# Optimization experiments

Hardware: AMD Instinct MI355X
Metric: run time of the kernel (lower is better)

The kernel has to match this reference:

```python
import jax, jax.numpy as jnp
import numpy as np

EPS = 1e-5
DIL = 2
PAD = 2  # dilation * (kernel_size - 1) // 2


def _conv(x, w, dil, pad):
    return jax.lax.conv_general_dilated(
        x, w, window_strides=(1, 1), padding=[(pad, pad), (pad, pad)],
        rhs_dilation=(dil, dil), dimension_numbers=('NCHW', 'OIHW', 'NCHW'))


def _bn(x, g, b):
    # BatchNorm2d in training mode: per-channel batch stats over (N,H,W)
    m = x.mean(axis=(0, 2, 3), keepdims=True)
    v = x.var(axis=(0, 2, 3), keepdims=True)
    return (x - m) * jax.lax.rsqrt(v + EPS) * g[None, :, None, None] + b[None, :, None, None]


def _deform_conv(x, offset, w, dil=DIL, pad=PAD):
    # torchvision deform_conv2d v1 (no modulation): offset [B, 2*K, H, W] with
    # channel ordering (dy_0, dx_0, dy_1, dx_1, ...), kernel tap k = ky*3 + kx.
    B, C, H, W = x.shape
    Co = w.shape[0]
    K = 9
    off = offset.reshape(B, K, 2, H, W)
    dy, dx = off[:, :, 0], off[:, :, 1]              # [B,K,H,W]
    kr = jnp.arange(3)
    kyy = (jnp.repeat(kr, 3) * dil - pad).astype(x.dtype)   # [K]
    kxx = (jnp.tile(kr, 3) * dil - pad).astype(x.dtype)     # [K]
    hg = jnp.arange(H, dtype=x.dtype)
    wg = jnp.arange(W, dtype=x.dtype)
    py = hg[None, None, :, None] + kyy[None, :, None, None] + dy   # [B,K,H,W]
    px = wg[None, None, None, :] + kxx[None, :, None, None] + dx   # [B,K,H,W]
    y0 = jnp.floor(py)
    x0 = jnp.floor(px)
    wy = py - y0   # [B,K,H,W]
    wx = px - x0
    y0i = y0.astype(jnp.int32)
    x0i = x0.astype(jnp.int32)
    x_flat = x.reshape(B, C, H * W)

    def corner(yi, xi):
        valid = ((yi >= 0) & (yi < H) & (xi >= 0) & (xi < W)).astype(x.dtype)  # [B,K,H,W]
        idx = jnp.clip(yi, 0, H - 1) * W + jnp.clip(xi, 0, W - 1)
        v = jax.vmap(lambda xb, ib: xb[:, ib])(x_flat, idx.reshape(B, -1))    # [B,C,K*H*W]
        return v.reshape(B, C, K, H, W) * valid[:, None]

    v00 = corner(y0i, x0i)
    v01 = corner(y0i, x0i + 1)
    v10 = corner(y0i + 1, x0i)
    v11 = corner(y0i + 1, x0i + 1)
    wy_ = wy[:, None]   # [B,1,K,H,W]
    wx_ = wx[:, None]
    sampled = (v00 * (1 - wy_) * (1 - wx_) + v01 * (1 - wy_) * wx_
               + v10 * wy_ * (1 - wx_) + v11 * wy_ * wx_)          # [B,C,K,H,W]
    return jnp.einsum('bckhw,ock->bohw', sampled, w.reshape(Co, C, K))


def setup_inputs() -> dict:
    key = jax.random.key(0)
    ks = jax.random.split(key, 4)
    B, C, H, W = 4, 256, 56, 56
    x = jax.random.normal(ks[0], (B, C, H, W), dtype=jnp.float32)
    w_off = jax.random.normal(ks[1], (18, C, 3, 3), dtype=jnp.float32) * 0.01
    b_off = jnp.zeros((18,), dtype=jnp.float32)
    w1 = jax.random.normal(ks[2], (C, C, 3, 3), dtype=jnp.float32) * (1.0 / np.sqrt(9 * C))
    w2 = jax.random.normal(ks[3], (C, C, 3, 3), dtype=jnp.float32) * (1.0 / np.sqrt(9 * C))
    gamma1 = jnp.ones((C,), dtype=jnp.float32)
    beta1 = jnp.zeros((C,), dtype=jnp.float32)
    gamma2 = jnp.ones((C,), dtype=jnp.float32)
    beta2 = jnp.zeros((C,), dtype=jnp.float32)
    return {'x': x, 'w_off': w_off, 'b_off': b_off, 'w1': w1, 'gamma1': gamma1,
            'beta1': beta1, 'w2': w2, 'gamma2': gamma2, 'beta2': beta2}


def reference(x, w_off, b_off, w1, gamma1, beta1, w2, gamma2, beta2):
    offset = _conv(x, w_off, DIL, PAD) + b_off[None, :, None, None]   # [B,18,H,W]
    out = _deform_conv(x, offset, w1)
    out = jax.nn.relu(_bn(out, gamma1, beta1))
    out = _conv(out, w2, 1, 1)
    out = _bn(out, gamma2, beta2)
    return jax.nn.relu(out + x)
```

## Files before the change

### kernel.cpp

```cpp
#include <hip/hip_runtime.h>

typedef __bf16 bf16;
typedef bf16 bf16x4 __attribute__((ext_vector_type(4)));
typedef bf16 bf16x8 __attribute__((ext_vector_type(8)));
typedef float f32x4 __attribute__((ext_vector_type(4)));

#define CH 256
#define HH 56
#define WW 56
#define HW 3136
#define MM 12544
#define KT 2304

__device__ __forceinline__ void gll16(const bf16* g, bf16* l) {
  __builtin_amdgcn_global_load_lds(
      (const __attribute__((address_space(1))) void*)g,
      (__attribute__((address_space(3))) void*)l, 16, 0, 0);
}

template <int N>
__device__ __forceinline__ void waitvm() {
  if constexpr (N == 0) asm volatile("s_waitcnt vmcnt(0)" ::: "memory");
  else if constexpr (N == 3) asm volatile("s_waitcnt vmcnt(3)" ::: "memory");
  else if constexpr (N == 4) asm volatile("s_waitcnt vmcnt(4)" ::: "memory");
}

__global__ __launch_bounds__(256) void nchw2nhwc_k(const float* __restrict__ x,
                                                   bf16* __restrict__ o) {
  __shared__ float t[32][33];
  const int b = blockIdx.z, hw0 = blockIdx.x * 32, c0 = blockIdx.y * 32;
  const int tid = threadIdx.x;
  {
    const int cl = tid >> 3, hwl = (tid & 7) * 4;
    f32x4 v = *(const f32x4*)&x[(size_t)(b * CH + c0 + cl) * HW + hw0 + hwl];
#pragma unroll
    for (int i = 0; i < 4; ++i) t[cl][hwl + i] = v[i];
  }
  __syncthreads();
  const int hwl = tid >> 3, cl = (tid & 7) * 4;
  bf16x4 ov;
#pragma unroll
  for (int i = 0; i < 4; ++i) ov[i] = (bf16)t[cl + i][hwl];
  *(bf16x4*)&o[(size_t)(b * HW + hw0 + hwl) * CH + c0 + cl] = ov;
}

__global__ void reorder_all_k(const float* __restrict__ w1,
                              const float* __restrict__ w2,
                              const float* __restrict__ woff,
                              bf16* __restrict__ w1t, bf16* __restrict__ w2t,
                              bf16* __restrict__ wof) {
  const int gid = blockIdx.x;
  if (gid < 4608) {
    const int idx = gid * 256 + threadIdx.x;
    const float* in = (gid < 2304) ? w1 : w2;
    bf16* out = (gid < 2304) ? w1t : w2t;
    const int li = (gid < 2304) ? idx : idx - 2304 * 256;
    const int o = li / KT, r = li - o * KT;
    const int k = r >> 8, c = r & 255;
    out[li] = (bf16)in[(size_t)(o * CH + c) * 9 + k];
  } else {
    const int li = (gid - 4608) * 256 + threadIdx.x;
    const int o = li / KT, r = li - o * KT;
    const int k = r >> 8, c = r & 255;
    wof[li] = (bf16)((o < 18) ? woff[(size_t)(o * CH + c) * 9 + k] : 0.f);
  }
}

__global__ __launch_bounds__(256) void build_deform_k(
    const bf16* __restrict__ xn, const float* __restrict__ offb,
    const float* __restrict__ boff, bf16* __restrict__ A1) {
  const int tid = threadIdx.x;
  const int m = blockIdx.x * 16 + (tid >> 4);
  const int l15 = tid & 15;
  const int b = m / HW, hw = m - b * HW;
  const int h = hw / WW, w = hw - h * WW;
  const float* orow = offb + m * 18;
  const bf16* xb = xn + (size_t)b * HW * CH;
  bf16* dst = A1 + (size_t)m * KT;
  for (int tap = 0; tap < 9; ++tap) {
    const int ky = tap / 3, kx = tap - ky * 3;
    const float dy = orow[2 * tap] + boff[2 * tap];
    const float dx = orow[2 * tap + 1] + boff[2 * tap + 1];
    const float py = (float)(h + ky * 2 - 2) + dy;
    const float px = (float)(w + kx * 2 - 2) + dx;
    const float y0f = floorf(py), x0f = floorf(px);
    const int y0 = (int)y0f, x0 = (int)x0f;
    const float wy = py - y0f, wx = px - x0f;
    const float w00 = (1.f - wy) * (1.f - wx), w01 = (1.f - wy) * wx;
    const float w10 = wy * (1.f - wx), w11 = wy * wx;
    const bool vy0 = (unsigned)y0 < HH, vy1 = (unsigned)(y0 + 1) < HH;
    const bool vx0 = (unsigned)x0 < WW, vx1 = (unsigned)(x0 + 1) < WW;
    const bf16* p00 = xb + (long long)(y0 * WW + x0) * CH;
#pragma unroll
    for (int j = 0; j < 2; ++j) {
      const int cc = j * 128 + l15 * 8;
      bf16x8 v00 = {}, v01 = {}, v10 = {}, v11 = {};
      if (vy0 && vx0) v00 = *(const bf16x8*)(p00 + cc);
      if (vy0 && vx1) v01 = *(const bf16x8*)(p00 + CH + cc);
      if (vy1 && vx0) v10 = *(const bf16x8*)(p00 + WW * CH + cc);
      if (vy1 && vx1) v11 = *(const bf16x8*)(p00 + WW * CH + CH + cc);
      bf16x8 o;
#pragma unroll
      for (int i = 0; i < 8; ++i)
        o[i] = (bf16)(w00 * (float)v00[i] + w01 * (float)v01[i] +
                      w10 * (float)v10[i] + w11 * (float)v11[i]);
      *(bf16x8*)(dst + tap * 256 + cc) = o;
    }
  }
}

template <int MODE, int EPI, int SWZ, int TN, int KS>
__global__ __launch_bounds__(256, 3) void gemm_k(
    const bf16* __restrict__ Asrc, const bf16* __restrict__ Bt,
    const bf16* __restrict__ zp, bf16* __restrict__ outb,
    float* __restrict__ sS, float* __restrict__ sQ,
    float* __restrict__ offout, const int dil, const int pad) {
  constexpr int PB = TN / 32;
  constexpr int NF = TN / 32;
  constexpr int SL = 2 + PB;
  __shared__ __align__(16) bf16 Ab[2][4096];
  __shared__ __align__(16) bf16 Bb[2][TN * 64];
  const int tid = threadIdx.x;
  int n0, m0;
  if (SWZ) {
    const int gid = blockIdx.x;
    const int swz = (gid & 7) * 98 + (gid >> 3);
    n0 = (swz & 3) * 64;
    m0 = (swz >> 2) * 64;
  } else {
    n0 = blockIdx.x * TN;
    m0 = blockIdx.y * 64;
  }
  const int kbase = blockIdx.z * KS * 64;
  const int lane = tid & 63, wv = tid >> 6;
  const int wrM = wv >> 1, wcN = wv & 1;
  const int fr = lane & 15, kg = lane >> 4;
  const int srow = tid >> 3, cpos = tid & 7;
  const int sxor = (cpos ^ (srow & 7)) * 8;

  int bb[2], hh[2], wwv[2];
  const bf16* aptr[2];
  if (MODE == 1) {
#pragma unroll
    for (int pa = 0; pa < 2; ++pa) {
      const int m = m0 + pa * 32 + srow;
      bb[pa] = m / HW;
      const int hw = m - bb[pa] * HW;
      hh[pa] = hw / WW;
      wwv[pa] = hw - hh[pa] * WW;
    }
  } else {
#pragma unroll
    for (int pa = 0; pa < 2; ++pa)
      aptr[pa] = Asrc + (size_t)(m0 + pa * 32 + srow) * KT + kbase + sxor;
  }
  const bf16* bptr[PB];
#pragma unroll
  for (int pb = 0; pb < PB; ++pb)
    bptr[pb] = Bt + (size_t)(n0 + pb * 32 + srow) * KT + kbase + sxor;

  f32x4 acc[2][NF] = {};

  auto STAGE = [&](int kt, int buf) {
    const int kk = kbase + kt * 64;
#pragma unroll
    for (int pa = 0; pa < 2; ++pa) {
      const bf16* as;
      if (MODE == 0) {
        as = aptr[pa] + kt * 64;
      } else {
        const int tap = kk >> 8, coff = kk & 255;
        const int ky = tap / 3, kx = tap - ky * 3;
        const int y = hh[pa] + ky * dil - pad, xx = wwv[pa] + kx * dil - pad;
        const bool ok = ((unsigned)y < HH) && ((unsigned)xx < WW);
        as = ok ? Asrc + ((size_t)(bb[pa] * HW + y * WW + xx) * CH + coff + sxor)
                : zp + sxor;
      }
      gll16(as, &Ab[buf][(pa * 32 + srow) * 64 + cpos * 8]);
    }
#pragma unroll
    for (int pb = 0; pb < PB; ++pb)
      gll16(bptr[pb] + kt * 64, &Bb[buf][(pb * 32 + srow) * 64 + cpos * 8]);
  };

  auto COMPUTE = [&](int buf) {
#pragma unroll
    for (int kh = 0; kh < 2; ++kh) {
      bf16x8 af[2], bv[NF];
#pragma unroll
      for (int mf = 0; mf < 2; ++mf) {
        const int row = wrM * 32 + mf * 16 + fr;
        const int g = (kh * 4 + kg) ^ (row & 7);
        af[mf] = *(const bf16x8*)&Ab[buf][row * 64 + g * 8];
      }
#pragma unroll
      for (int nf = 0; nf < NF; ++nf) {
        const int row = wcN * (NF * 16) + nf * 16 + fr;
        const int g = (kh * 4 + kg) ^ (row & 7);
        bv[nf] = *(const bf16x8*)&Bb[buf][row * 64 + g * 8];
      }
#pragma unroll
      for (int mf = 0; mf < 2; ++mf)
#pragma unroll
        for (int nf = 0; nf < NF; ++nf)
          acc[mf][nf] = __builtin_amdgcn_mfma_f32_16x16x32_bf16(af[mf], bv[nf],
                                                                acc[mf][nf], 0, 0, 0);
    }
  };

  STAGE(0, 0);
  STAGE(1, 1);
  int buf = 0;
  for (int kt = 0; kt < KS; ++kt) {
    if (kt + 1 < KS) waitvm<SL>();
    else waitvm<0>();
    __builtin_amdgcn_s_barrier();
    __builtin_amdgcn_sched_barrier(0);
    COMPUTE(buf);
    __builtin_amdgcn_sched_barrier(0);
    __builtin_amdgcn_s_barrier();
    if (kt + 2 < KS) STAGE(kt + 2, buf);
    buf ^= 1;
  }

  if constexpr (EPI == 1) {
#pragma unroll
    for (int mf = 0; mf < 2; ++mf) {
      const int rr = m0 + wrM * 32 + mf * 16 + kg * 4;
#pragma unroll
      for (int nf = 0; nf < NF; ++nf) {
        const int col = n0 + wcN * (NF * 16) + nf * 16 + fr;
#pragma unroll
        for (int r = 0; r < 4; ++r)
          outb[(size_t)(rr + r) * CH + col] = (bf16)acc[mf][nf][r];
      }
    }
    float ps[NF], pq[NF];
#pragma unroll
    for (int nf = 0; nf < NF; ++nf) {
      float s = 0.f, q = 0.f;
#pragma unroll
      for (int mf = 0; mf < 2; ++mf)
#pragma unroll
        for (int r = 0; r < 4; ++r) {
          const float v = acc[mf][nf][r];
          s += v;
          q += v * v;
        }
      s += __shfl_xor(s, 16);
      s += __shfl_xor(s, 32);
      q += __shfl_xor(q, 16);
      q += __shfl_xor(q, 32);
      ps[nf] = s;
      pq[nf] = q;
    }
    float* red = (float*)&Ab[0][0];
    if (tid < 128) red[tid] = 0.f;
    __syncthreads();
    if (kg == 0) {
#pragma unroll
      for (int nf = 0; nf < NF; ++nf) {
        const int cb = wcN * (NF * 16) + nf * 16 + fr;
        atomicAdd(&red[cb], ps[nf]);
        atomicAdd(&red[64 + cb], pq[nf]);
      }
    }
    __syncthreads();
    if (tid < 64) {
      atomicAdd(&sS[n0 + tid], red[tid]);
      atomicAdd(&sQ[n0 + tid], red[64 + tid]);
    }
  } else {
#pragma unroll
    for (int mf = 0; mf < 2; ++mf) {
      const int rr = m0 + wrM * 32 + mf * 16 + kg * 4;
#pragma unroll
      for (int nf = 0; nf < NF; ++nf) {
        const int col = n0 + wcN * (NF * 16) + nf * 16 + fr;
        if (col < 18) {
#pragma unroll
          for (int r = 0; r < 4; ++r)
            atomicAdd(&offout[(size_t)(rr + r) * 18 + col], acc[mf][nf][r]);
        }
      }
    }
  }
}

__global__ __launch_bounds__(256) void a1_kb(const bf16* __restrict__ in,
                                             const float* __restrict__ s,
                                             const float* __restrict__ sq,
                                             const float* __restrict__ g,
                                             const float* __restrict__ be,
                                             bf16* __restrict__ out) {
  const size_t idx = (size_t)(blockIdx.x * 256 + threadIdx.x) * 8;
  const int c0 = (int)(idx & 255);
  const float inv = 1.f / (float)MM;
  bf16x8 v = *(const bf16x8*)&in[idx];
  bf16x8 o;
#pragma unroll
  for (int i = 0; i < 8; ++i) {
    const int c = c0 + i;
    const float mean = s[c] * inv;
    const float var = sq[c] * inv - mean * mean;
    const float sc = g[c] * rsqrtf(var + 1e-5f);
    const float bi = be[c] - mean * sc;
    float r = (float)v[i] * sc + bi;
    o[i] = (bf16)(r > 0.f ? r : 0.f);
  }
  *(bf16x8*)&out[idx] = o;
}

__global__ __launch_bounds__(256) void final_kb(const bf16* __restrict__ o2,
                                                const float* __restrict__ x,
                                                const float* __restrict__ s,
                                                const float* __restrict__ sq,
                                                const float* __restrict__ g,
                                                const float* __restrict__ be,
                                                float* __restrict__ out) {
  __shared__ float t[32][33];
  const int b = blockIdx.z, hw0 = blockIdx.x * 32, o0 = blockIdx.y * 32;
  const int tid = threadIdx.x;
  {
    const int hwl = tid >> 3, ol = (tid & 7) * 4;
    bf16x4 v = *(const bf16x4*)&o2[(size_t)(b * HW + hw0 + hwl) * CH + o0 + ol];
#pragma unroll
    for (int i = 0; i < 4; ++i) t[ol + i][hwl] = (float)v[i];
  }
  __syncthreads();
  const int ol = tid >> 3, hwl = (tid & 7) * 4;
  const int ch = o0 + ol;
  const float inv = 1.f / (float)MM;
  const float mean = s[ch] * inv;
  const float var = sq[ch] * inv - mean * mean;
  const float sc = g[ch] * rsqrtf(var + 1e-5f);
  const float bb = be[ch] - mean * sc;
  const size_t xi = (size_t)(b * CH + ch) * HW + hw0 + hwl;
  f32x4 xv = *(const f32x4*)&x[xi];
  f32x4 r;
#pragma unroll
  for (int i = 0; i < 4; ++i) {
    float v = t[ol][hwl + i] * sc + bb + xv[i];
    r[i] = v > 0.f ? v : 0.f;
  }
  *(f32x4*)&out[xi] = r;
}

#define WS_XN 0ULL
#define WS_W1T 6422528ULL
#define WS_W2T 7602176ULL
#define WS_WOF 8781824ULL
#define WS_OFFB 9076736ULL
#define WS_A1 9979904ULL
#define WS_O1 67782656ULL
#define WS_ACT 74205184ULL
#define WS_O2 80627712ULL
#define WS_ZP 87050240ULL
#define WS_STAT 87054336ULL

extern "C" void kernel_launch(void* const* d_in, const int* in_sizes, int n_in,
                              void* d_out, int out_size, void* d_ws, size_t ws_size,
                              hipStream_t stream) {
  const float* x = (const float*)d_in[0];
  const float* w_off = (const float*)d_in[1];
  const float* b_off = (const float*)d_in[2];
  const float* w1 = (const float*)d_in[3];
  const float* g1 = (const float*)d_in[4];
  const float* be1 = (const float*)d_in[5];
  const float* w2 = (const float*)d_in[6];
  const float* g2 = (const float*)d_in[7];
  const float* be2 = (const float*)d_in[8];
  float* out = (float*)d_out;
  char* ws = (char*)d_ws;

  bf16* xn = (bf16*)(ws + WS_XN);
  bf16* w1t = (bf16*)(ws + WS_W1T);
  bf16* w2t = (bf16*)(ws + WS_W2T);
  bf16* wof = (bf16*)(ws + WS_WOF);
  float* offb = (float*)(ws + WS_OFFB);
  bf16* A1 = (bf16*)(ws + WS_A1);
  bf16* o1 = (bf16*)(ws + WS_O1);
  bf16* act = (bf16*)(ws + WS_ACT);
  bf16* o2 = (bf16*)(ws + WS_O2);
  bf16* zp = (bf16*)(ws + WS_ZP);
  float* s1 = (float*)(ws + WS_STAT);
  float* sq1 = (float*)(ws + WS_STAT + 1024);
  float* s2 = (float*)(ws + WS_STAT + 2048);
  float* sq2 = (float*)(ws + WS_STAT + 3072);

  hipMemsetAsync(ws + WS_ZP, 0, 8192, stream);
  hipMemsetAsync(ws + WS_OFFB, 0, 903168, stream);

  nchw2nhwc_k<<<dim3(98, 8, 4), 256, 0, stream>>>(x, xn);
  reorder_all_k<<<5184, 256, 0, stream>>>(w1, w2, w_off, w1t, w2t, wof);

  gemm_k<1, 0, 0, 32, 9><<<dim3(1, 196, 4), 256, 0, stream>>>(
      xn, wof, zp, nullptr, nullptr, nullptr, offb, 2, 2);

  build_deform_k<<<784, 256, 0, stream>>>(xn, offb, b_off, A1);

  gemm_k<0, 1, 1, 64, 36><<<dim3(784), 256, 0, stream>>>(
      A1, w1t, zp, o1, s1, sq1, nullptr, 0, 0);
  a1_kb<<<1568, 256, 0, stream>>>(o1, s1, sq1, g1, be1, act);

  gemm_k<1, 1, 1, 64, 36><<<dim3(784), 256, 0, stream>>>(
      act, w2t, zp, o2, s2, sq2, nullptr, 1, 1);

  final_kb<<<dim3(98, 8, 4), 256, 0, stream>>>(o2, x, s2, sq2, g2, be2, out);
}
```

Before: 203.9 us.

## Merge prep kernels, raise MFMA wave priority, precompute BN scale/bias in shared memory

```diff
diff --git a/kernel.cpp b/kernel.cpp
--- a/kernel.cpp
+++ b/kernel.cpp
@@ -25,41 +25,41 @@
   else if constexpr (N == 4) asm volatile("s_waitcnt vmcnt(4)" ::: "memory");
 }
 
-__global__ __launch_bounds__(256) void nchw2nhwc_k(const float* __restrict__ x,
-                                                   bf16* __restrict__ o) {
+__global__ __launch_bounds__(256) void prep_k(
+    const float* __restrict__ x, bf16* __restrict__ xn,
+    const float* __restrict__ w1, const float* __restrict__ w2,
+    const float* __restrict__ woff, bf16* __restrict__ w1t,
+    bf16* __restrict__ w2t, bf16* __restrict__ wof) {
   __shared__ float t[32][33];
-  const int b = blockIdx.z, hw0 = blockIdx.x * 32, c0 = blockIdx.y * 32;
+  const int gid = blockIdx.x;
   const int tid = threadIdx.x;
-  {
-    const int cl = tid >> 3, hwl = (tid & 7) * 4;
-    f32x4 v = *(const f32x4*)&x[(size_t)(b * CH + c0 + cl) * HW + hw0 + hwl];
-#pragma unroll
-    for (int i = 0; i < 4; ++i) t[cl][hwl + i] = v[i];
-  }
-  __syncthreads();
-  const int hwl = tid >> 3, cl = (tid & 7) * 4;
-  bf16x4 ov;
-#pragma unroll
-  for (int i = 0; i < 4; ++i) ov[i] = (bf16)t[cl + i][hwl];
-  *(bf16x4*)&o[(size_t)(b * HW + hw0 + hwl) * CH + c0 + cl] = ov;
-}
-
-__global__ void reorder_all_k(const float* __restrict__ w1,
-                              const float* __restrict__ w2,
-                              const float* __restrict__ woff,
-                              bf16* __restrict__ w1t, bf16* __restrict__ w2t,
-                              bf16* __restrict__ wof) {
-  const int gid = blockIdx.x;
-  if (gid < 4608) {
-    const int idx = gid * 256 + threadIdx.x;
-    const float* in = (gid < 2304) ? w1 : w2;
-    bf16* out = (gid < 2304) ? w1t : w2t;
-    const int li = (gid < 2304) ? idx : idx - 2304 * 256;
+  if (gid < 3136) {
+    const int bx = gid % 98, r = gid / 98;
+    const int by = r & 7, b = r >> 3;
+    const int hw0 = bx * 32, c0 = by * 32;
+    {
+      const int cl = tid >> 3, hwl = (tid & 7) * 4;
+      f32x4 v = *(const f32x4*)&x[(size_t)(b * CH + c0 + cl) * HW + hw0 + hwl];
+#pragma unroll
+      for (int i = 0; i < 4; ++i) t[cl][hwl + i] = v[i];
+    }
+    __syncthreads();
+    const int hwl = tid >> 3, cl = (tid & 7) * 4;
+    bf16x4 ov;
+#pragma unroll
+    for (int i = 0; i < 4; ++i) ov[i] = (bf16)t[cl + i][hwl];
+    *(bf16x4*)&xn[(size_t)(b * HW + hw0 + hwl) * CH + c0 + cl] = ov;
+  } else if (gid < 3136 + 4608) {
+    const int g2 = gid - 3136;
+    const int idx = g2 * 256 + tid;
+    const float* in = (g2 < 2304) ? w1 : w2;
+    bf16* out = (g2 < 2304) ? w1t : w2t;
+    const int li = (g2 < 2304) ? idx : idx - 2304 * 256;
     const int o = li / KT, r = li - o * KT;
     const int k = r >> 8, c = r & 255;
     out[li] = (bf16)in[(size_t)(o * CH + c) * 9 + k];
   } else {
-    const int li = (gid - 4608) * 256 + threadIdx.x;
+    const int li = (gid - 3136 - 4608) * 256 + tid;
     const int o = li / KT, r = li - o * KT;
     const int k = r >> 8, c = r & 255;
     wof[li] = (bf16)((o < 18) ? woff[(size_t)(o * CH + c) * 9 + k] : 0.f);
@@ -199,12 +199,14 @@
         const int g = (kh * 4 + kg) ^ (row & 7);
         bv[nf] = *(const bf16x8*)&Bb[buf][row * 64 + g * 8];
       }
+      __builtin_amdgcn_s_setprio(1);
 #pragma unroll
       for (int mf = 0; mf < 2; ++mf)
 #pragma unroll
         for (int nf = 0; nf < NF; ++nf)
           acc[mf][nf] = __builtin_amdgcn_mfma_f32_16x16x32_bf16(af[mf], bv[nf],
                                                                 acc[mf][nf], 0, 0, 0);
+      __builtin_amdgcn_s_setprio(0);
     }
   };
 
@@ -293,19 +295,24 @@
                                              const float* __restrict__ g,
                                              const float* __restrict__ be,
                                              bf16* __restrict__ out) {
-  const size_t idx = (size_t)(blockIdx.x * 256 + threadIdx.x) * 8;
+  __shared__ float scs[256], bis[256];
+  const int tid = threadIdx.x;
+  {
+    const float inv = 1.f / (float)MM;
+    const float mean = s[tid] * inv;
+    const float var = sq[tid] * inv - mean * mean;
+    const float sc = g[tid] * rsqrtf(var + 1e-5f);
+    scs[tid] = sc;
+    bis[tid] = be[tid] - mean * sc;
+  }
+  __syncthreads();
+  const size_t idx = (size_t)(blockIdx.x * 256 + tid) * 8;
   const int c0 = (int)(idx & 255);
-  const float inv = 1.f / (float)MM;
   bf16x8 v = *(const bf16x8*)&in[idx];
   bf16x8 o;
 #pragma unroll
   for (int i = 0; i < 8; ++i) {
-    const int c = c0 + i;
-    const float mean = s[c] * inv;
-    const float var = sq[c] * inv - mean * mean;
-    const float sc = g[c] * rsqrtf(var + 1e-5f);
-    const float bi = be[c] - mean * sc;
-    float r = (float)v[i] * sc + bi;
+    float r = (float)v[i] * scs[c0 + i] + bis[c0 + i];
     o[i] = (bf16)(r > 0.f ? r : 0.f);
   }
   *(bf16x8*)&out[idx] = o;
@@ -391,8 +398,7 @@
   hipMemsetAsync(ws + WS_ZP, 0, 8192, stream);
   hipMemsetAsync(ws + WS_OFFB, 0, 903168, stream);
 
-  nchw2nhwc_k<<<dim3(98, 8, 4), 256, 0, stream>>>(x, xn);
-  reorder_all_k<<<5184, 256, 0, stream>>>(w1, w2, w_off, w1t, w2t, wof);
+  prep_k<<<8320, 256, 0, stream>>>(x, xn, w1, w2, w_off, w1t, w2t, wof);
 
   gemm_k<1, 0, 0, 32, 9><<<dim3(1, 196, 4), 256, 0, stream>>>(
       xn, wof, zp, nullptr, nullptr, nullptr, offb, 2, 2);
```

Measured after the change: 197.6 us, median of 2. 1.03x faster.
